# Optimization experiments

Hardware: AMD Instinct MI355X
Metric: run time of the kernel (lower is better)

Reference implementation:

```python
import jax, jax.numpy as jnp
import numpy as np
import math

B, L, D, P = 2, 2048, 256, 32

def _lin_init(key, fan_in, shape):
    return jax.random.normal(key, shape, dtype=jnp.float32) / np.float32(math.sqrt(fan_in))

def setup_inputs() -> dict:
    key = jax.random.key(0)
    ks = jax.random.split(key, 16)
    return {
        "x": jax.random.normal(ks[0], (B, L, D), dtype=jnp.float32),
        "pos_phases": jax.random.normal(ks[1], (L, P), dtype=jnp.float32) * np.float32(math.pi),
        "w_pos_value": _lin_init(ks[2], D, (D, D)), "b_pos_value": jnp.zeros((D,), jnp.float32),
        "w_key": _lin_init(ks[3], D, (D, P)), "b_key": jnp.zeros((P,), jnp.float32),
        "w_kv": _lin_init(ks[4], D, (D, D)), "b_kv": jnp.zeros((D,), jnp.float32),
        "w_vg1": _lin_init(ks[5], 2 * D, (2 * D, D)), "b_vg1": jnp.zeros((D,), jnp.float32),
        "w_vg2": _lin_init(ks[6], D, (D, 1)), "b_vg2": jnp.zeros((1,), jnp.float32),
        "w_bg1": _lin_init(ks[7], D, (D, D // 2)), "b_bg1": jnp.zeros((D // 2,), jnp.float32),
        "w_bg2": _lin_init(ks[8], D // 2, (D // 2, 2)), "b_bg2": jnp.zeros((2,), jnp.float32),
        "ln_r_g": jnp.ones((D,), jnp.float32), "ln_r_b": jnp.zeros((D,), jnp.float32),
        "w_r1": _lin_init(ks[9], D, (D, 2 * D)), "b_r1": jnp.zeros((2 * D,), jnp.float32),
        "w_r2": _lin_init(ks[10], 2 * D, (2 * D, D)), "b_r2": jnp.zeros((D,), jnp.float32),
        "ln_o_g": jnp.ones((D,), jnp.float32), "ln_o_b": jnp.zeros((D,), jnp.float32),
        "w_out": _lin_init(ks[11], D, (D, D)), "b_out": jnp.zeros((D,), jnp.float32),
    }

def _ln(z, g, b, eps=1e-5):
    mu = z.mean(-1, keepdims=True)
    var = ((z - mu) ** 2).mean(-1, keepdims=True)
    return (z - mu) * jax.lax.rsqrt(var + eps) * g + b

def _shift1(z):
    # torch.roll(shifts=1, dims=1) then zero first position == shift right with zero pad
    return jnp.concatenate([jnp.zeros_like(z[:, :1]), z[:, :-1]], axis=1)

def reference(x, pos_phases, w_pos_value, b_pos_value, w_key, b_key, w_kv, b_kv,
              w_vg1, b_vg1, w_vg2, b_vg2, w_bg1, b_bg1, w_bg2, b_bg2,
              ln_r_g, ln_r_b, w_r1, b_r1, w_r2, b_r2, ln_o_g, ln_o_b, w_out, b_out):
    Bv, Lv, Dv = x.shape
    Pv = pos_phases.shape[1]
    inv_sqrt_p = np.float32(1.0 / math.sqrt(Pv))

    # --- positional memory ---
    pos_phasors = jnp.exp(1j * pos_phases)                      # (L,P) complex64
    pos_values = (x @ w_pos_value + b_pos_value).astype(jnp.complex64)  # (B,L,D)
    pos_bound = pos_phasors[None, :, :, None] * pos_values[:, :, None, :]  # (B,L,P,D)
    pos_memory = jnp.cumsum(pos_bound, axis=1)
    pos_query = jnp.exp(-1j * pos_phases)                       # (L,P)
    pos_retrieved = (pos_memory * pos_query[None, :, :, None]).sum(axis=2).real * inv_sqrt_p

    # --- content-based KV memory ---
    key_phases = jnp.tanh(x @ w_key + b_key) * np.float32(math.pi)  # (B,L,P)
    key_phasors = jnp.exp(1j * key_phases)
    kv_values = (x @ w_kv + b_kv).astype(jnp.complex64)         # (B,L,D)

    x_shifted = _shift1(x)
    gate_input = jnp.concatenate([x, x_shifted], axis=-1)       # (B,L,2D)
    h = jax.nn.gelu(gate_input @ w_vg1 + b_vg1, approximate=False)
    value_gates = jax.nn.sigmoid(h @ w_vg2 + b_vg2)             # (B,L,1)

    key_phasors_shifted = _shift1(key_phasors)                  # (B,L,P)
    kv_bound = (key_phasors_shifted[..., None] * kv_values[:, :, None, :]) \
               * value_gates[:, :, :, None].astype(jnp.complex64)  # (B,L,P,D)
    kv_memory = jnp.cumsum(kv_bound, axis=1)
    gate_cumsum = jnp.maximum(jnp.cumsum(value_gates, axis=1), 1.0)  # (B,L,1)
    kv_query = jnp.exp(-1j * key_phases)                        # (B,L,P)
    kv_retrieved = (kv_memory * kv_query[..., None]).sum(axis=2).real
    kv_retrieved = kv_retrieved / (jnp.sqrt(gate_cumsum) * np.float32(math.sqrt(Pv)))

    # --- blend, refine, output ---
    bg_h = jax.nn.gelu(x @ w_bg1 + b_bg1, approximate=False)
    blend = jax.nn.softmax(bg_h @ w_bg2 + b_bg2, axis=-1)       # (B,L,2)
    blended = blend[..., 0:1] * pos_retrieved + blend[..., 1:2] * kv_retrieved

    refined = jax.nn.gelu(_ln(blended, ln_r_g, ln_r_b) @ w_r1 + b_r1, approximate=False) @ w_r2 + b_r2
    return x + (_ln(refined, ln_o_g, ln_o_b) @ w_out + b_out)
```

## Files before the change

### kernel.cpp

```cpp
#include <hip/hip_runtime.h>
#include <math.h>

#define B_ 2
#define L_ 2048
#define D_ 256
#define P_ 32
#define NC_ 64
#define CL_ 32

#define INV_SQRT_P 0.17677669529663687f
#define PI_F 3.14159265358979323846f

typedef __attribute__((ext_vector_type(8))) short bf16x8;
typedef __attribute__((ext_vector_type(4))) float f32x4;

__device__ __forceinline__ float gelu_exact(float x){
    return 0.5f * x * (1.0f + erff(x * 0.70710678118654752f));
}

__device__ __forceinline__ unsigned short f2bf(float f){
    unsigned int u = __float_as_uint(f);
    u += 0x7FFFu + ((u >> 16) & 1u);
    return (unsigned short)(u >> 16);
}

__global__ __launch_bounds__(256) void k_prep(
    const float* __restrict__ x, const float* __restrict__ pos_phases,
    const float* __restrict__ w_pv, const float* __restrict__ w_kv,
    const float* __restrict__ w_vg1, const float* __restrict__ w_bg1,
    const float* __restrict__ w_r1, const float* __restrict__ w_r2,
    const float* __restrict__ w_out, const float* __restrict__ w_key,
    unsigned short* __restrict__ wq, unsigned short* __restrict__ xbf,
    unsigned short* __restrict__ xsbf,
    float* __restrict__ cpos, float* __restrict__ spos)
{
    int id = blockIdx.x * 256 + threadIdx.x;
    if (id < 630784){
        const float* src; int N; int local;
        if (id < 65536)       { src = w_pv;  N = 256; local = id; }
        else if (id < 131072) { src = w_kv;  N = 256; local = id - 65536; }
        else if (id < 262144) { src = w_vg1; N = 256; local = id - 131072; }
        else if (id < 294912) { src = w_bg1; N = 128; local = id - 262144; }
        else if (id < 425984) { src = w_r1;  N = 512; local = id - 294912; }
        else if (id < 557056) { src = w_r2;  N = 256; local = id - 425984; }
        else if (id < 622592) { src = w_out; N = 256; local = id - 557056; }
        else                  { src = w_key; N = 32;  local = id - 622592; }
        int j = local & 7, lane = (local >> 3) & 63, tile = local >> 9;
        int NT = N >> 4;
        int nt = tile % NT, kt = tile / NT;
        int row = kt * 32 + ((lane >> 4) << 3) + j;
        int col = nt * 16 + (lane & 15);
        wq[id] = f2bf(src[(size_t)row * N + col]);
    } else if (id < 2727936){
        int id2 = id - 630784;
        int shifted = id2 >> 20;
        int local = id2 & 1048575;
        int j = local & 7, lane = (local >> 3) & 63;
        int kt = (local >> 9) & 7, lt = (local >> 12) & 127, b = local >> 19;
        int k = kt * 32 + ((lane >> 4) << 3) + j;
        int l = lt * 16 + (lane & 15);
        float v;
        if (shifted) v = (l >= 1) ? x[(size_t)(b * L_ + l - 1) * D_ + k] : 0.0f;
        else         v = x[(size_t)(b * L_ + l) * D_ + k];
        (shifted ? xsbf : xbf)[local] = f2bf(v);
    } else {
        int idx = id - 2727936;
        float s, c;
        sincosf(pos_phases[idx], &s, &c);
        cpos[idx] = c;
        spos[idx] = s;
    }
}

__global__ __launch_bounds__(512) void k_proj(
    const unsigned short* __restrict__ wq,
    const float* __restrict__ b_pv, const float* __restrict__ b_kv,
    const float* __restrict__ b_vg1,
    const float* __restrict__ w_vg2, const float* __restrict__ b_vg2,
    const float* __restrict__ b_bg1,
    const float* __restrict__ w_bg2, const float* __restrict__ b_bg2,
    const float* __restrict__ b_key,
    const unsigned short* __restrict__ xbf, const unsigned short* __restrict__ xsbf,
    float* __restrict__ pv, float* __restrict__ kvv,
    float* __restrict__ ck, float* __restrict__ sk,
    float* __restrict__ vg, float* __restrict__ blend0, float* __restrict__ blend1)
{
    __shared__ float hbuf[16][257];
    __shared__ float bhbuf[16][129];
    __shared__ float kph[16][33];
    __shared__ float red[16][17], red2[16][17], red3[16][17];

    const int i = threadIdx.x;
    const int lane = i & 63, w = i >> 6;
    const int b = blockIdx.x >> 7, lt = blockIdx.x & 127, l0 = lt * 16;
    const int g = lane >> 4, c = lane & 15;

    bf16x8 xa[8], xs[8];
    {
        const unsigned short* base  = xbf  + (size_t)((b * 128 + lt) * 8) * 512 + lane * 8;
        const unsigned short* bases = xsbf + (size_t)((b * 128 + lt) * 8) * 512 + lane * 8;
        #pragma unroll
        for (int kt = 0; kt < 8; ++kt){
            xa[kt] = *(const bf16x8*)(base  + kt * 512);
            xs[kt] = *(const bf16x8*)(bases + kt * 512);
        }
    }

    const unsigned short* wpv  = wq;
    const unsigned short* wkv  = wq + 65536;
    const unsigned short* wvg1 = wq + 131072;
    const unsigned short* wbg1 = wq + 262144;
    const unsigned short* wkey = wq + 622592;

    for (int jb = w; jb < 58; jb += 8){
        f32x4 acc = {0.f, 0.f, 0.f, 0.f};
        if (jb < 2){
            int nt = jb;
            #pragma unroll
            for (int kt = 0; kt < 8; ++kt){
                bf16x8 bf = *(const bf16x8*)(wkey + (kt * 2 + nt) * 512 + lane * 8);
                acc = __builtin_amdgcn_mfma_f32_16x16x32_bf16(xa[kt], bf, acc, 0, 0, 0);
            }
            float bb = b_key[nt * 16 + c];
            #pragma unroll
            for (int r = 0; r < 4; ++r)
                kph[4 * g + r][nt * 16 + c] = acc[r] + bb;
        } else if (jb < 18){
            int nt = jb - 2;
            #pragma unroll
            for (int kt = 0; kt < 8; ++kt){
                bf16x8 bf = *(const bf16x8*)(wpv + (kt * 16 + nt) * 512 + lane * 8);
                acc = __builtin_amdgcn_mfma_f32_16x16x32_bf16(xa[kt], bf, acc, 0, 0, 0);
            }
            float bb = b_pv[nt * 16 + c];
            #pragma unroll
            for (int r = 0; r < 4; ++r)
                pv[(size_t)(b * L_ + l0 + 4 * g + r) * D_ + nt * 16 + c] = acc[r] + bb;
        } else if (jb < 34){
            int nt = jb - 18;
            #pragma unroll
            for (int kt = 0; kt < 8; ++kt){
                bf16x8 bf = *(const bf16x8*)(wkv + (kt * 16 + nt) * 512 + lane * 8);
                acc = __builtin_amdgcn_mfma_f32_16x16x32_bf16(xa[kt], bf, acc, 0, 0, 0);
            }
            float bb = b_kv[nt * 16 + c];
            #pragma unroll
            for (int r = 0; r < 4; ++r)
                kvv[(size_t)(b * L_ + l0 + 4 * g + r) * D_ + nt * 16 + c] = acc[r] + bb;
        } else if (jb < 50){
            int nt = jb - 34;
            #pragma unroll
            for (int kt = 0; kt < 8; ++kt){
                bf16x8 bf = *(const bf16x8*)(wvg1 + (kt * 16 + nt) * 512 + lane * 8);
                acc = __builtin_amdgcn_mfma_f32_16x16x32_bf16(xa[kt], bf, acc, 0, 0, 0);
            }
            #pragma unroll
            for (int kt = 8; kt < 16; ++kt){
                bf16x8 bf = *(const bf16x8*)(wvg1 + (kt * 16 + nt) * 512 + lane * 8);
                acc = __builtin_amdgcn_mfma_f32_16x16x32_bf16(xs[kt - 8], bf, acc, 0, 0, 0);
            }
            float bb = b_vg1[nt * 16 + c];
            #pragma unroll
            for (int r = 0; r < 4; ++r)
                hbuf[4 * g + r][nt * 16 + c] = gelu_exact(acc[r] + bb);
        } else {
            int nt = jb - 50;
            #pragma unroll
            for (int kt = 0; kt < 8; ++kt){
                bf16x8 bf = *(const bf16x8*)(wbg1 + (kt * 8 + nt) * 512 + lane * 8);
                acc = __builtin_amdgcn_mfma_f32_16x16x32_bf16(xa[kt], bf, acc, 0, 0, 0);
            }
            float bb = b_bg1[nt * 16 + c];
            #pragma unroll
            for (int r = 0; r < 4; ++r)
                bhbuf[4 * g + r][nt * 16 + c] = gelu_exact(acc[r] + bb);
        }
    }
    __syncthreads();

    {
        int t = i >> 5, p = i & 31;
        float a = tanhf(kph[t][p]) * PI_F;
        float s, cc;
        sincosf(a, &s, &cc);
        ck[(size_t)(b * L_ + l0 + t) * P_ + p] = cc;
        sk[(size_t)(b * L_ + l0 + t) * P_ + p] = s;
    }

    if (i < 256){
        int t = i >> 4, c2 = i & 15;
        float s = 0.f;
        #pragma unroll
        for (int m = 0; m < 16; ++m){ int dd = c2 + 16 * m; s += hbuf[t][dd] * w_vg2[dd]; }
        red[t][c2] = s;
    } else {
        int ii = i - 256;
        int t = ii >> 4, c2 = ii & 15;
        float s0 = 0.f, s1 = 0.f;
        #pragma unroll
        for (int m = 0; m < 8; ++m){
            int jj = c2 + 16 * m;
            float v = bhbuf[t][jj];
            s0 += v * w_bg2[jj * 2 + 0];
            s1 += v * w_bg2[jj * 2 + 1];
        }
        red2[t][c2] = s0; red3[t][c2] = s1;
    }
    __syncthreads();
    if (i < 16){
        float s = 0.f;
        #pragma unroll
        for (int c2 = 0; c2 < 16; ++c2) s += red[i][c2];
        s += b_vg2[0];
        vg[b * L_ + l0 + i] = 1.0f / (1.0f + expf(-s));
    } else if (i < 32){
        int t = i - 16;
        float s0 = 0.f, s1 = 0.f;
        #pragma unroll
        for (int c2 = 0; c2 < 16; ++c2){ s0 += red2[t][c2]; s1 += red3[t][c2]; }
        s0 += b_bg2[0]; s1 += b_bg2[1];
        float mx = fmaxf(s0, s1);
        float e0 = expf(s0 - mx), e1 = expf(s1 - mx);
        float inv = 1.0f / (e0 + e1);
        blend0[b * L_ + l0 + t] = e0 * inv;
        blend1[b * L_ + l0 + t] = e1 * inv;
    }
}

__global__ __launch_bounds__(128) void k_scan1(
    const float* __restrict__ cpos, const float* __restrict__ spos,
    const float* __restrict__ ck, const float* __restrict__ sk,
    const float* __restrict__ pv, const float* __restrict__ kvv,
    const float* __restrict__ vg,
    float* __restrict__ posSr, float* __restrict__ posSi,
    float* __restrict__ kvSr, float* __restrict__ kvSi,
    float* __restrict__ rnorm)
{
    const int z = blockIdx.z;
    const int c = blockIdx.x, b = blockIdx.y;
    const int i = threadIdx.x;
    if (z == 16){
        if (c != 0) return;
        float loc[16];
        float run = 0.f;
        #pragma unroll
        for (int m = 0; m < 16; ++m){ run += vg[b * L_ + i * 16 + m]; loc[m] = run; }
        __shared__ float part[128];
        part[i] = run;
        __syncthreads();
        for (int off = 1; off < 128; off <<= 1){
            float t = (i >= off) ? part[i - off] : 0.0f;
            __syncthreads();
            part[i] += t;
            __syncthreads();
        }
        float excl = part[i] - run;
        #pragma unroll
        for (int m = 0; m < 16; ++m){
            float gc = fmaxf(excl + loc[m], 1.0f);
            rnorm[b * L_ + i * 16 + m] = rsqrtf(gc) * INV_SQRT_P;
        }
        return;
    }
    const int type = z >> 3, pg = (z >> 1) & 3, dhalf = z & 1;
    const int d = dhalf * 128 + i;
    const int p0 = pg * 8;
    float Sr[8], Si[8];
    #pragma unroll
    for (int j = 0; j < 8; ++j){ Sr[j] = 0.f; Si[j] = 0.f; }

    if (type == 0){
        for (int l = 0; l < CL_; ++l){
            int row = c * CL_ + l;
            float v = pv[(size_t)(b * L_ + row) * D_ + d];
            float4 c0 = *(const float4*)(cpos + row * P_ + p0);
            float4 c1 = *(const float4*)(cpos + row * P_ + p0 + 4);
            float4 s0 = *(const float4*)(spos + row * P_ + p0);
            float4 s1 = *(const float4*)(spos + row * P_ + p0 + 4);
            Sr[0] = fmaf(c0.x, v, Sr[0]); Si[0] = fmaf(s0.x, v, Si[0]);
            Sr[1] = fmaf(c0.y, v, Sr[1]); Si[1] = fmaf(s0.y, v, Si[1]);
            Sr[2] = fmaf(c0.z, v, Sr[2]); Si[2] = fmaf(s0.z, v, Si[2]);
            Sr[3] = fmaf(c0.w, v, Sr[3]); Si[3] = fmaf(s0.w, v, Si[3]);
            Sr[4] = fmaf(c1.x, v, Sr[4]); Si[4] = fmaf(s1.x, v, Si[4]);
            Sr[5] = fmaf(c1.y, v, Sr[5]); Si[5] = fmaf(s1.y, v, Si[5]);
            Sr[6] = fmaf(c1.z, v, Sr[6]); Si[6] = fmaf(s1.z, v, Si[6]);
            Sr[7] = fmaf(c1.w, v, Sr[7]); Si[7] = fmaf(s1.w, v, Si[7]);
        }
        #pragma unroll
        for (int j = 0; j < 8; ++j){
            size_t o = (size_t)((b * NC_ + c) * P_ + p0 + j) * D_ + d;
            posSr[o] = Sr[j]; posSi[o] = Si[j];
        }
    } else {
        float pc[8], ps[8];
        int srow = c * CL_ - 1;
        if (srow >= 0){
            float4 c0 = *(const float4*)(ck + ((size_t)b * L_ + srow) * P_ + p0);
            float4 c1 = *(const float4*)(ck + ((size_t)b * L_ + srow) * P_ + p0 + 4);
            float4 s0 = *(const float4*)(sk + ((size_t)b * L_ + srow) * P_ + p0);
            float4 s1 = *(const float4*)(sk + ((size_t)b * L_ + srow) * P_ + p0 + 4);
            pc[0]=c0.x; pc[1]=c0.y; pc[2]=c0.z; pc[3]=c0.w;
            pc[4]=c1.x; pc[5]=c1.y; pc[6]=c1.z; pc[7]=c1.w;
            ps[0]=s0.x; ps[1]=s0.y; ps[2]=s0.z; ps[3]=s0.w;
            ps[4]=s1.x; ps[5]=s1.y; ps[6]=s1.z; ps[7]=s1.w;
        } else {
            #pragma unroll
            for (int j = 0; j < 8; ++j){ pc[j] = 0.f; ps[j] = 0.f; }
        }
        for (int l = 0; l < CL_; ++l){
            int row = c * CL_ + l;
            float vv = kvv[(size_t)(b * L_ + row) * D_ + d] * vg[b * L_ + row];
            float4 c0 = *(const float4*)(ck + ((size_t)b * L_ + row) * P_ + p0);
            float4 c1 = *(const float4*)(ck + ((size_t)b * L_ + row) * P_ + p0 + 4);
            float4 s0 = *(const float4*)(sk + ((size_t)b * L_ + row) * P_ + p0);
            float4 s1 = *(const float4*)(sk + ((size_t)b * L_ + row) * P_ + p0 + 4);
            #pragma unroll
            for (int j = 0; j < 8; ++j){
                Sr[j] = fmaf(pc[j], vv, Sr[j]);
                Si[j] = fmaf(ps[j], vv, Si[j]);
            }
            pc[0]=c0.x; pc[1]=c0.y; pc[2]=c0.z; pc[3]=c0.w;
            pc[4]=c1.x; pc[5]=c1.y; pc[6]=c1.z; pc[7]=c1.w;
            ps[0]=s0.x; ps[1]=s0.y; ps[2]=s0.z; ps[3]=s0.w;
            ps[4]=s1.x; ps[5]=s1.y; ps[6]=s1.z; ps[7]=s1.w;
        }
        #pragma unroll
        for (int j = 0; j < 8; ++j){
            size_t o = (size_t)((b * NC_ + c) * P_ + p0 + j) * D_ + d;
            kvSr[o] = Sr[j]; kvSi[o] = Si[j];
        }
    }
}

__global__ __launch_bounds__(256) void k_prefix(
    float* __restrict__ posSr, float* __restrict__ posSi,
    float* __restrict__ kvSr, float* __restrict__ kvSi)
{
    int gid = blockIdx.x * 256 + threadIdx.x;
    float* A = (gid < 16384) ? posSr : (gid < 32768) ? posSi
             : (gid < 49152) ? kvSr : kvSi;
    int g = gid & 16383;
    int b = g >> 13;
    int pd = g & 8191;
    float run = 0.f;
    #pragma unroll 4
    for (int cc = 0; cc < NC_; ++cc){
        size_t idx = (size_t)(b * NC_ + cc) * (P_ * D_) + pd;
        float t = A[idx];
        A[idx] = run;
        run += t;
    }
}

__global__ __launch_bounds__(256) void k_retrieve(
    const float* __restrict__ cpos, const float* __restrict__ spos,
    const float* __restrict__ ck, const float* __restrict__ sk,
    const float* __restrict__ pv, const float* __restrict__ kvv,
    const float* __restrict__ vg, const float* __restrict__ rnorm,
    const float* __restrict__ posSr, const float* __restrict__ posSi,
    const float* __restrict__ kvSr, const float* __restrict__ kvSi,
    float* __restrict__ posret, float* __restrict__ kvret)
{
    const int z = blockIdx.z;
    const int c = blockIdx.x, b = blockIdx.y;
    const int type = z >> 2, dquad = z & 3;
    const int lane = threadIdx.x & 63, wv = threadIdx.x >> 6;
    const int pg = lane >> 4, dl = lane & 15;
    const int d = dquad * 64 + wv * 16 + dl;
    const int p0 = pg * 8;

    float Sr[8], Si[8];

    if (type == 0){
        #pragma unroll
        for (int j = 0; j < 8; ++j){
            size_t o = (size_t)((b * NC_ + c) * P_ + p0 + j) * D_ + d;
            Sr[j] = posSr[o]; Si[j] = posSi[o];
        }
        for (int l = 0; l < CL_; ++l){
            int row = c * CL_ + l;
            float v = pv[(size_t)(b * L_ + row) * D_ + d];
            float4 c0 = *(const float4*)(cpos + row * P_ + p0);
            float4 c1 = *(const float4*)(cpos + row * P_ + p0 + 4);
            float4 s0 = *(const float4*)(spos + row * P_ + p0);
            float4 s1 = *(const float4*)(spos + row * P_ + p0 + 4);
            float r0 = 0.f, r1 = 0.f, r2 = 0.f, r3 = 0.f;
            Sr[0] = fmaf(c0.x, v, Sr[0]); r0 = fmaf(c0.x, Sr[0], r0);
            Si[0] = fmaf(s0.x, v, Si[0]); r1 = fmaf(s0.x, Si[0], r1);
            Sr[1] = fmaf(c0.y, v, Sr[1]); r2 = fmaf(c0.y, Sr[1], r2);
            Si[1] = fmaf(s0.y, v, Si[1]); r3 = fmaf(s0.y, Si[1], r3);
            Sr[2] = fmaf(c0.z, v, Sr[2]); r0 = fmaf(c0.z, Sr[2], r0);
            Si[2] = fmaf(s0.z, v, Si[2]); r1 = fmaf(s0.z, Si[2], r1);
            Sr[3] = fmaf(c0.w, v, Sr[3]); r2 = fmaf(c0.w, Sr[3], r2);
            Si[3] = fmaf(s0.w, v, Si[3]); r3 = fmaf(s0.w, Si[3], r3);
            Sr[4] = fmaf(c1.x, v, Sr[4]); r0 = fmaf(c1.x, Sr[4], r0);
            Si[4] = fmaf(s1.x, v, Si[4]); r1 = fmaf(s1.x, Si[4], r1);
            Sr[5] = fmaf(c1.y, v, Sr[5]); r2 = fmaf(c1.y, Sr[5], r2);
            Si[5] = fmaf(s1.y, v, Si[5]); r3 = fmaf(s1.y, Si[5], r3);
            Sr[6] = fmaf(c1.z, v, Sr[6]); r0 = fmaf(c1.z, Sr[6], r0);
            Si[6] = fmaf(s1.z, v, Si[6]); r1 = fmaf(s1.z, Si[6], r1);
            Sr[7] = fmaf(c1.w, v, Sr[7]); r2 = fmaf(c1.w, Sr[7], r2);
            Si[7] = fmaf(s1.w, v, Si[7]); r3 = fmaf(s1.w, Si[7], r3);
            float r = (r0 + r1) + (r2 + r3);
            r += __shfl_xor(r, 16, 64);
            r += __shfl_xor(r, 32, 64);
            if (pg == 0)
                posret[(size_t)(b * L_ + row) * D_ + d] = r * INV_SQRT_P;
        }
    } else {
        #pragma unroll
        for (int j = 0; j < 8; ++j){
            size_t o = (size_t)((b * NC_ + c) * P_ + p0 + j) * D_ + d;
            Sr[j] = kvSr[o]; Si[j] = kvSi[o];
        }
        float pc[8], ps[8];
        int srow = c * CL_ - 1;
        if (srow >= 0){
            float4 c0 = *(const float4*)(ck + ((size_t)b * L_ + srow) * P_ + p0);
            float4 c1 = *(const float4*)(ck + ((size_t)b * L_ + srow) * P_ + p0 + 4);
            float4 s0 = *(const float4*)(sk + ((size_t)b * L_ + srow) * P_ + p0);
            float4 s1 = *(const float4*)(sk + ((size_t)b * L_ + srow) * P_ + p0 + 4);
            pc[0]=c0.x; pc[1]=c0.y; pc[2]=c0.z; pc[3]=c0.w;
            pc[4]=c1.x; pc[5]=c1.y; pc[6]=c1.z; pc[7]=c1.w;
            ps[0]=s0.x; ps[1]=s0.y; ps[2]=s0.z; ps[3]=s0.w;
            ps[4]=s1.x; ps[5]=s1.y; ps[6]=s1.z; ps[7]=s1.w;
        } else {
            #pragma unroll
            for (int j = 0; j < 8; ++j){ pc[j] = 0.f; ps[j] = 0.f; }
        }
        for (int l = 0; l < CL_; ++l){
            int row = c * CL_ + l;
            float vv = kvv[(size_t)(b * L_ + row) * D_ + d] * vg[b * L_ + row];
            float rn = rnorm[b * L_ + row];
            float4 c0 = *(const float4*)(ck + ((size_t)b * L_ + row) * P_ + p0);
            float4 c1 = *(const float4*)(ck + ((size_t)b * L_ + row) * P_ + p0 + 4);
            float4 s0 = *(const float4*)(sk + ((size_t)b * L_ + row) * P_ + p0);
            float4 s1 = *(const float4*)(sk + ((size_t)b * L_ + row) * P_ + p0 + 4);
            float qc[8], qs[8];
            qc[0]=c0.x; qc[1]=c0.y; qc[2]=c0.z; qc[3]=c0.w;
            qc[4]=c1.x; qc[5]=c1.y; qc[6]=c1.z; qc[7]=c1.w;
            qs[0]=s0.x; qs[1]=s0.y; qs[2]=s0.z; qs[3]=s0.w;
            qs[4]=s1.x; qs[5]=s1.y; qs[6]=s1.z; qs[7]=s1.w;
            float r0 = 0.f, r1 = 0.f, r2 = 0.f, r3 = 0.f;
            #pragma unroll
            for (int j = 0; j < 8; ++j){
                Sr[j] = fmaf(pc[j], vv, Sr[j]);
                Si[j] = fmaf(ps[j], vv, Si[j]);
                if (j & 1){ r2 = fmaf(qc[j], Sr[j], r2); r3 = fmaf(qs[j], Si[j], r3); }
                else      { r0 = fmaf(qc[j], Sr[j], r0); r1 = fmaf(qs[j], Si[j], r1); }
                pc[j] = qc[j]; ps[j] = qs[j];
            }
            float r = (r0 + r1) + (r2 + r3);
            r += __shfl_xor(r, 16, 64);
            r += __shfl_xor(r, 32, 64);
            if (pg == 0)
                kvret[(size_t)(b * L_ + row) * D_ + d] = r * rn;
        }
    }
}

__global__ __launch_bounds__(512) void k_final(
    const float* __restrict__ x,
    const float* __restrict__ posret, const float* __restrict__ kvret,
    const float* __restrict__ blend0, const float* __restrict__ blend1,
    const unsigned short* __restrict__ wq,
    const float* __restrict__ ln_r_g, const float* __restrict__ ln_r_b,
    const float* __restrict__ b_r1, const float* __restrict__ b_r2,
    const float* __restrict__ ln_o_g, const float* __restrict__ ln_o_b,
    const float* __restrict__ b_out,
    float* __restrict__ out)
{
    __shared__ float zbuf[16][257];
    __shared__ __align__(16) unsigned short aA[8][512];
    __shared__ __align__(16) unsigned short aH[16][512];
    __shared__ float red[16][17], red2[16][17];
    __shared__ float mu[16], rs[16];

    const int i = threadIdx.x, lane = i & 63, w = i >> 6;
    const int b = blockIdx.x >> 7, l0 = (blockIdx.x & 127) * 16;
    const int g = lane >> 4, c = lane & 15;
    const unsigned short* wr1  = wq + 294912;
    const unsigned short* wr2  = wq + 425984;
    const unsigned short* wout = wq + 557056;

    {
        int t = i >> 5, c0 = (i & 31) * 8;
        size_t base = (size_t)(b * L_ + l0 + t) * D_ + c0;
        float w0 = blend0[b * L_ + l0 + t], w1 = blend1[b * L_ + l0 + t];
        #pragma unroll
        for (int m = 0; m < 8; ++m)
            zbuf[t][c0 + m] = w0 * posret[base + m] + w1 * kvret[base + m];
    }
    __syncthreads();

    if (i < 256){
        int t = i >> 4, c2 = i & 15;
        float s = 0.f, s2 = 0.f;
        #pragma unroll
        for (int m = 0; m < 16; ++m){ float v = zbuf[t][c2 + 16 * m]; s += v; s2 += v * v; }
        red[t][c2] = s; red2[t][c2] = s2;
    }
    __syncthreads();
    if (i < 16){
        float s = 0.f, s2 = 0.f;
        #pragma unroll
        for (int c2 = 0; c2 < 16; ++c2){ s += red[i][c2]; s2 += red2[i][c2]; }
        float mean = s * (1.0f / 256.0f);
        float var  = s2 * (1.0f / 256.0f) - mean * mean;
        mu[i] = mean; rs[i] = rsqrtf(var + 1e-5f);
    }
    __syncthreads();

    {
        int kt = i >> 6;
        int t2 = lane & 15, kb = kt * 32 + ((lane >> 4) << 3);
        float m_ = mu[t2], r_ = rs[t2];
        bf16x8 v8;
        #pragma unroll
        for (int j = 0; j < 8; ++j){
            int k = kb + j;
            float v = (zbuf[t2][k] - m_) * r_ * ln_r_g[k] + ln_r_b[k];
            v8[j] = (short)f2bf(v);
        }
        *(bf16x8*)&aA[kt][lane * 8] = v8;
    }
    __syncthreads();

    {
        bf16x8 afr[8];
        #pragma unroll
        for (int kt = 0; kt < 8; ++kt) afr[kt] = *(const bf16x8*)&aA[kt][lane * 8];
        for (int q = 0; q < 4; ++q){
            int nt = w + 8 * q;
            f32x4 acc = {0.f, 0.f, 0.f, 0.f};
            #pragma unroll
            for (int kt = 0; kt < 8; ++kt){
                bf16x8 bf = *(const bf16x8*)(wr1 + (kt * 32 + nt) * 512 + lane * 8);
                acc = __builtin_amdgcn_mfma_f32_16x16x32_bf16(afr[kt], bf, acc, 0, 0, 0);
            }
            float bb = b_r1[nt * 16 + c];
            #pragma unroll
            for (int r = 0; r < 4; ++r){
                float hv = gelu_exact(acc[r] + bb);
                int t = 4 * g + r, hcol = nt * 16 + c;
                int kt2 = hcol >> 5, kk = hcol & 31;
                int lane2 = ((kk >> 3) << 4) + t, j2 = kk & 7;
                aH[kt2][lane2 * 8 + j2] = f2bf(hv);
            }
        }
    }
    __syncthreads();

    {
        bf16x8 hfr[16];
        #pragma unroll
        for (int kt = 0; kt < 16; ++kt) hfr[kt] = *(const bf16x8*)&aH[kt][lane * 8];
        for (int q = 0; q < 2; ++q){
            int nt = w + 8 * q;
            f32x4 acc = {0.f, 0.f, 0.f, 0.f};
            #pragma unroll
            for (int kt = 0; kt < 16; ++kt){
                bf16x8 bf = *(const bf16x8*)(wr2 + (kt * 16 + nt) * 512 + lane * 8);
                acc = __builtin_amdgcn_mfma_f32_16x16x32_bf16(hfr[kt], bf, acc, 0, 0, 0);
            }
            float bb = b_r2[nt * 16 + c];
            #pragma unroll
            for (int r = 0; r < 4; ++r)
                zbuf[4 * g + r][nt * 16 + c] = acc[r] + bb;
        }
    }
    __syncthreads();

    if (i < 256){
        int t = i >> 4, c2 = i & 15;
        float s = 0.f, s2 = 0.f;
        #pragma unroll
        for (int m = 0; m < 16; ++m){ float v = zbuf[t][c2 + 16 * m]; s += v; s2 += v * v; }
        red[t][c2] = s; red2[t][c2] = s2;
    }
    __syncthreads();
    if (i < 16){
        float s = 0.f, s2 = 0.f;
        #pragma unroll
        for (int c2 = 0; c2 < 16; ++c2){ s += red[i][c2]; s2 += red2[i][c2]; }
        float mean = s * (1.0f / 256.0f);
        float var  = s2 * (1.0f / 256.0f) - mean * mean;
        mu[i] = mean; rs[i] = rsqrtf(var + 1e-5f);
    }
    __syncthreads();

    {
        int kt = i >> 6;
        int t2 = lane & 15, kb = kt * 32 + ((lane >> 4) << 3);
        float m_ = mu[t2], r_ = rs[t2];
        bf16x8 v8;
        #pragma unroll
        for (int j = 0; j < 8; ++j){
            int k = kb + j;
            float v = (zbuf[t2][k] - m_) * r_ * ln_o_g[k] + ln_o_b[k];
            v8[j] = (short)f2bf(v);
        }
        *(bf16x8*)&aA[kt][lane * 8] = v8;
    }
    __syncthreads();

    {
        bf16x8 azr[8];
        #pragma unroll
        for (int kt = 0; kt < 8; ++kt) azr[kt] = *(const bf16x8*)&aA[kt][lane * 8];
        for (int q = 0; q < 2; ++q){
            int nt = w + 8 * q;
            f32x4 acc = {0.f, 0.f, 0.f, 0.f};
            #pragma unroll
            for (int kt = 0; kt < 8; ++kt){
                bf16x8 bf = *(const bf16x8*)(wout + (kt * 16 + nt) * 512 + lane * 8);
                acc = __builtin_amdgcn_mfma_f32_16x16x32_bf16(azr[kt], bf, acc, 0, 0, 0);
            }
            float bb = b_out[nt * 16 + c];
            #pragma unroll
            for (int r = 0; r < 4; ++r){
                size_t o = (size_t)(b * L_ + l0 + 4 * g + r) * D_ + nt * 16 + c;
                out[o] = x[o] + acc[r] + bb;
            }
        }
    }
}

extern "C" void kernel_launch(void* const* d_in, const int* in_sizes, int n_in,
                              void* d_out, int out_size, void* d_ws, size_t ws_size,
                              hipStream_t stream) {
    const float* x          = (const float*)d_in[0];
    const float* pos_phases = (const float*)d_in[1];
    const float* w_pv       = (const float*)d_in[2];
    const float* b_pv       = (const float*)d_in[3];
    const float* w_key      = (const float*)d_in[4];
    const float* b_key      = (const float*)d_in[5];
    const float* w_kv       = (const float*)d_in[6];
    const float* b_kv       = (const float*)d_in[7];
    const float* w_vg1      = (const float*)d_in[8];
    const float* b_vg1      = (const float*)d_in[9];
    const float* w_vg2      = (const float*)d_in[10];
    const float* b_vg2      = (const float*)d_in[11];
    const float* w_bg1      = (const float*)d_in[12];
    const float* b_bg1      = (const float*)d_in[13];
    const float* w_bg2      = (const float*)d_in[14];
    const float* b_bg2      = (const float*)d_in[15];
    const float* ln_r_g     = (const float*)d_in[16];
    const float* ln_r_b     = (const float*)d_in[17];
    const float* w_r1       = (const float*)d_in[18];
    const float* b_r1       = (const float*)d_in[19];
    const float* w_r2       = (const float*)d_in[20];
    const float* b_r2       = (const float*)d_in[21];
    const float* ln_o_g     = (const float*)d_in[22];
    const float* ln_o_b     = (const float*)d_in[23];
    const float* w_out      = (const float*)d_in[24];
    const float* b_out      = (const float*)d_in[25];
    float* out = (float*)d_out;

    float* ws = (float*)d_ws;
    size_t off = 0;
    float* cpos   = ws + off; off += (size_t)L_ * P_;
    float* spos   = ws + off; off += (size_t)L_ * P_;
    float* pv     = ws + off; off += (size_t)B_ * L_ * D_;
    float* kvv    = ws + off; off += (size_t)B_ * L_ * D_;
    float* ck     = ws + off; off += (size_t)B_ * L_ * P_;
    float* sk     = ws + off; off += (size_t)B_ * L_ * P_;
    float* vg     = ws + off; off += (size_t)B_ * L_;
    float* rnorm  = ws + off; off += (size_t)B_ * L_;
    float* blend0 = ws + off; off += (size_t)B_ * L_;
    float* blend1 = ws + off; off += (size_t)B_ * L_;
    float* posret = ws + off; off += (size_t)B_ * L_ * D_;
    float* kvret  = ws + off; off += (size_t)B_ * L_ * D_;
    float* posSr  = ws + off; off += (size_t)B_ * NC_ * P_ * D_;
    float* posSi  = ws + off; off += (size_t)B_ * NC_ * P_ * D_;
    float* kvSr   = ws + off; off += (size_t)B_ * NC_ * P_ * D_;
    float* kvSi   = ws + off; off += (size_t)B_ * NC_ * P_ * D_;
    unsigned short* wq   = (unsigned short*)(ws + off); off += 630784 / 2;
    unsigned short* xbf  = (unsigned short*)(ws + off); off += 1048576 / 2;
    unsigned short* xsbf = (unsigned short*)(ws + off); off += 1048576 / 2;

    k_prep<<<10912, 256, 0, stream>>>(x, pos_phases,
        w_pv, w_kv, w_vg1, w_bg1, w_r1, w_r2, w_out, w_key,
        wq, xbf, xsbf, cpos, spos);

    k_proj<<<B_ * 128, 512, 0, stream>>>(wq,
        b_pv, b_kv, b_vg1, w_vg2, b_vg2, b_bg1, w_bg2, b_bg2, b_key,
        xbf, xsbf,
        pv, kvv, ck, sk, vg, blend0, blend1);

    k_scan1<<<dim3(NC_, B_, 17), 128, 0, stream>>>(cpos, spos, ck, sk, pv, kvv, vg,
                                                   posSr, posSi, kvSr, kvSi, rnorm);

    k_prefix<<<256, 256, 0, stream>>>(posSr, posSi, kvSr, kvSi);

    k_retrieve<<<dim3(NC_, B_, 8), 256, 0, stream>>>(cpos, spos, ck, sk, pv, kvv,
                                                     vg, rnorm,
                                                     posSr, posSi, kvSr, kvSi,
                                                     posret, kvret);

    k_final<<<B_ * 128, 512, 0, stream>>>(x, posret, kvret, blend0, blend1, wq,
        ln_r_g, ln_r_b, b_r1, b_r2, ln_o_g, ln_o_b, b_out, out);
}
```

Measured before the change: 94.20 us.

## Fuse x bf16 conversion into projection, widen scan blocks, parallelize chunk prefix

Removes the separate bf16 packing of x and shifted x from the prep kernel. The projection kernel now reads fp32 x directly and converts it into MFMA fragments in registers, which drops a global write and read round trip. The chunk-summary scan now uses 256-thread blocks covering all D per block, halving the z-dimension grid. The chunk prefix kernel switches to a segmented float4 scan with shared-memory totals, so four threads split the 64 chunks instead of one thread walking them serially.

```diff
diff --git a/kernel.cpp b/kernel.cpp
--- a/kernel.cpp
+++ b/kernel.cpp
@@ -25,13 +25,12 @@
 }
 
 __global__ __launch_bounds__(256) void k_prep(
-    const float* __restrict__ x, const float* __restrict__ pos_phases,
+    const float* __restrict__ pos_phases,
     const float* __restrict__ w_pv, const float* __restrict__ w_kv,
     const float* __restrict__ w_vg1, const float* __restrict__ w_bg1,
     const float* __restrict__ w_r1, const float* __restrict__ w_r2,
     const float* __restrict__ w_out, const float* __restrict__ w_key,
-    unsigned short* __restrict__ wq, unsigned short* __restrict__ xbf,
-    unsigned short* __restrict__ xsbf,
+    unsigned short* __restrict__ wq,
     float* __restrict__ cpos, float* __restrict__ spos)
 {
     int id = blockIdx.x * 256 + threadIdx.x;
@@ -51,20 +50,8 @@
         int row = kt * 32 + ((lane >> 4) << 3) + j;
         int col = nt * 16 + (lane & 15);
         wq[id] = f2bf(src[(size_t)row * N + col]);
-    } else if (id < 2727936){
-        int id2 = id - 630784;
-        int shifted = id2 >> 20;
-        int local = id2 & 1048575;
-        int j = local & 7, lane = (local >> 3) & 63;
-        int kt = (local >> 9) & 7, lt = (local >> 12) & 127, b = local >> 19;
-        int k = kt * 32 + ((lane >> 4) << 3) + j;
-        int l = lt * 16 + (lane & 15);
-        float v;
-        if (shifted) v = (l >= 1) ? x[(size_t)(b * L_ + l - 1) * D_ + k] : 0.0f;
-        else         v = x[(size_t)(b * L_ + l) * D_ + k];
-        (shifted ? xsbf : xbf)[local] = f2bf(v);
     } else {
-        int idx = id - 2727936;
+        int idx = id - 630784;
         float s, c;
         sincosf(pos_phases[idx], &s, &c);
         cpos[idx] = c;
@@ -73,6 +60,7 @@
 }
 
 __global__ __launch_bounds__(512) void k_proj(
+    const float* __restrict__ x,
     const unsigned short* __restrict__ wq,
     const float* __restrict__ b_pv, const float* __restrict__ b_kv,
     const float* __restrict__ b_vg1,
@@ -80,7 +68,6 @@
     const float* __restrict__ b_bg1,
     const float* __restrict__ w_bg2, const float* __restrict__ b_bg2,
     const float* __restrict__ b_key,
-    const unsigned short* __restrict__ xbf, const unsigned short* __restrict__ xsbf,
     float* __restrict__ pv, float* __restrict__ kvv,
     float* __restrict__ ck, float* __restrict__ sk,
     float* __restrict__ vg, float* __restrict__ blend0, float* __restrict__ blend1)
@@ -97,12 +84,41 @@
 
     bf16x8 xa[8], xs[8];
     {
-        const unsigned short* base  = xbf  + (size_t)((b * 128 + lt) * 8) * 512 + lane * 8;
-        const unsigned short* bases = xsbf + (size_t)((b * 128 + lt) * 8) * 512 + lane * 8;
+        int row  = l0 + (lane & 15);
+        int rowp = row - 1;
+        const float* xr = x + (size_t)(b * L_ + row) * D_ + ((lane >> 4) << 3);
         #pragma unroll
         for (int kt = 0; kt < 8; ++kt){
-            xa[kt] = *(const bf16x8*)(base  + kt * 512);
-            xs[kt] = *(const bf16x8*)(bases + kt * 512);
+            float4 a0 = *(const float4*)(xr + kt * 32);
+            float4 a1 = *(const float4*)(xr + kt * 32 + 4);
+            bf16x8 v;
+            v[0] = (short)f2bf(a0.x); v[1] = (short)f2bf(a0.y);
+            v[2] = (short)f2bf(a0.z); v[3] = (short)f2bf(a0.w);
+            v[4] = (short)f2bf(a1.x); v[5] = (short)f2bf(a1.y);
+            v[6] = (short)f2bf(a1.z); v[7] = (short)f2bf(a1.w);
+            xa[kt] = v;
+        }
+        if (rowp >= 0){
+            const float* xp = x + (size_t)(b * L_ + rowp) * D_ + ((lane >> 4) << 3);
+            #pragma unroll
+            for (int kt = 0; kt < 8; ++kt){
+                float4 a0 = *(const float4*)(xp + kt * 32);
+                float4 a1 = *(const float4*)(xp + kt * 32 + 4);
+                bf16x8 v;
+                v[0] = (short)f2bf(a0.x); v[1] = (short)f2bf(a0.y);
+                v[2] = (short)f2bf(a0.z); v[3] = (short)f2bf(a0.w);
+                v[4] = (short)f2bf(a1.x); v[5] = (short)f2bf(a1.y);
+                v[6] = (short)f2bf(a1.z); v[7] = (short)f2bf(a1.w);
+                xs[kt] = v;
+            }
+        } else {
+            #pragma unroll
+            for (int kt = 0; kt < 8; ++kt){
+                bf16x8 v;
+                #pragma unroll
+                for (int j = 0; j < 8; ++j) v[j] = 0;
+                xs[kt] = v;
+            }
         }
     }
 
@@ -227,7 +243,7 @@
     }
 }
 
-__global__ __launch_bounds__(128) void k_scan1(
+__global__ __launch_bounds__(256) void k_scan1(
     const float* __restrict__ cpos, const float* __restrict__ spos,
     const float* __restrict__ ck, const float* __restrict__ sk,
     const float* __restrict__ pv, const float* __restrict__ kvv,
@@ -239,16 +255,16 @@
     const int z = blockIdx.z;
     const int c = blockIdx.x, b = blockIdx.y;
     const int i = threadIdx.x;
-    if (z == 16){
+    if (z == 8){
         if (c != 0) return;
-        float loc[16];
+        float loc[8];
         float run = 0.f;
         #pragma unroll
-        for (int m = 0; m < 16; ++m){ run += vg[b * L_ + i * 16 + m]; loc[m] = run; }
-        __shared__ float part[128];
+        for (int m = 0; m < 8; ++m){ run += vg[b * L_ + i * 8 + m]; loc[m] = run; }
+        __shared__ float part[256];
         part[i] = run;
         __syncthreads();
-        for (int off = 1; off < 128; off <<= 1){
+        for (int off = 1; off < 256; off <<= 1){
             float t = (i >= off) ? part[i - off] : 0.0f;
             __syncthreads();
             part[i] += t;
@@ -256,14 +272,14 @@
         }
         float excl = part[i] - run;
         #pragma unroll
-        for (int m = 0; m < 16; ++m){
+        for (int m = 0; m < 8; ++m){
             float gc = fmaxf(excl + loc[m], 1.0f);
-            rnorm[b * L_ + i * 16 + m] = rsqrtf(gc) * INV_SQRT_P;
+            rnorm[b * L_ + i * 8 + m] = rsqrtf(gc) * INV_SQRT_P;
         }
         return;
     }
-    const int type = z >> 3, pg = (z >> 1) & 3, dhalf = z & 1;
-    const int d = dhalf * 128 + i;
+    const int type = z >> 2, pg = z & 3;
+    const int d = i;
     const int p0 = pg * 8;
     float Sr[8], Si[8];
     #pragma unroll
@@ -336,19 +352,40 @@
     float* __restrict__ posSr, float* __restrict__ posSi,
     float* __restrict__ kvSr, float* __restrict__ kvSi)
 {
-    int gid = blockIdx.x * 256 + threadIdx.x;
-    float* A = (gid < 16384) ? posSr : (gid < 32768) ? posSi
-             : (gid < 49152) ? kvSr : kvSi;
-    int g = gid & 16383;
-    int b = g >> 13;
-    int pd = g & 8191;
-    float run = 0.f;
-    #pragma unroll 4
-    for (int cc = 0; cc < NC_; ++cc){
-        size_t idx = (size_t)(b * NC_ + cc) * (P_ * D_) + pd;
-        float t = A[idx];
-        A[idx] = run;
-        run += t;
+    __shared__ float4 tot_s[64][4];
+    const int colLocal = threadIdx.x >> 2, seg = threadIdx.x & 3;
+    const int col = blockIdx.x * 64 + colLocal;
+    const int a = col >> 12;
+    const int rem = col & 4095;
+    const int b = rem >> 11;
+    const int pd = (rem & 2047) * 4;
+    float* A = (a == 0) ? posSr : (a == 1) ? posSi : (a == 2) ? kvSr : kvSi;
+    float* base = A + (size_t)b * NC_ * (P_ * D_) + pd;
+
+    float4 t[16];
+    #pragma unroll
+    for (int k = 0; k < 16; ++k)
+        t[k] = *(const float4*)(base + (size_t)(seg * 16 + k) * (P_ * D_));
+    float4 tot = {0.f, 0.f, 0.f, 0.f};
+    #pragma unroll
+    for (int k = 0; k < 16; ++k){
+        tot.x += t[k].x; tot.y += t[k].y; tot.z += t[k].z; tot.w += t[k].w;
+    }
+    tot_s[colLocal][seg] = tot;
+    __syncthreads();
+    float4 run = {0.f, 0.f, 0.f, 0.f};
+    #pragma unroll
+    for (int s = 0; s < 3; ++s){
+        if (s < seg){
+            float4 v = tot_s[colLocal][s];
+            run.x += v.x; run.y += v.y; run.z += v.z; run.w += v.w;
+        }
+    }
+    #pragma unroll
+    for (int k = 0; k < 16; ++k){
+        float4 cur = t[k];
+        *(float4*)(base + (size_t)(seg * 16 + k) * (P_ * D_)) = run;
+        run.x += cur.x; run.y += cur.y; run.z += cur.z; run.w += cur.w;
     }
 }
 
@@ -675,21 +712,18 @@
     float* posSi  = ws + off; off += (size_t)B_ * NC_ * P_ * D_;
     float* kvSr   = ws + off; off += (size_t)B_ * NC_ * P_ * D_;
     float* kvSi   = ws + off; off += (size_t)B_ * NC_ * P_ * D_;
-    unsigned short* wq   = (unsigned short*)(ws + off); off += 630784 / 2;
-    unsigned short* xbf  = (unsigned short*)(ws + off); off += 1048576 / 2;
-    unsigned short* xsbf = (unsigned short*)(ws + off); off += 1048576 / 2;
-
-    k_prep<<<10912, 256, 0, stream>>>(x, pos_phases,
+    unsigned short* wq = (unsigned short*)(ws + off); off += 630784 / 2;
+
+    k_prep<<<2720, 256, 0, stream>>>(pos_phases,
         w_pv, w_kv, w_vg1, w_bg1, w_r1, w_r2, w_out, w_key,
-        wq, xbf, xsbf, cpos, spos);
-
-    k_proj<<<B_ * 128, 512, 0, stream>>>(wq,
+        wq, cpos, spos);
+
+    k_proj<<<B_ * 128, 512, 0, stream>>>(x, wq,
         b_pv, b_kv, b_vg1, w_vg2, b_vg2, b_bg1, w_bg2, b_bg2, b_key,
-        xbf, xsbf,
         pv, kvv, ck, sk, vg, blend0, blend1);
 
-    k_scan1<<<dim3(NC_, B_, 17), 128, 0, stream>>>(cpos, spos, ck, sk, pv, kvv, vg,
-                                                   posSr, posSi, kvSr, kvSi, rnorm);
+    k_scan1<<<dim3(NC_, B_, 9), 256, 0, stream>>>(cpos, spos, ck, sk, pv, kvv, vg,
+                                                  posSr, posSi, kvSr, kvSi, rnorm);
 
     k_prefix<<<256, 256, 0, stream>>>(posSr, posSi, kvSr, kvSi);
 
```

New measurement: 89.07 us. 5.4% less time.
